# Kernel tuning notes

Hardware: AMD Instinct MI355X
Metric: run time of the kernel (lower is better)

The kernel has to match this reference:

```python
import jax, jax.numpy as jnp
import numpy as np

K, C, H, W, B = 128, 128, 24, 8, 32
HW = H * W
EPS = 1e-5


def setup_inputs() -> dict:
    key = jax.random.key(0)
    ks = jax.random.split(key, 4)
    feature = jax.random.normal(ks[0], (B, C, H, W), dtype=jnp.float32)
    target = jax.random.randint(ks[1], (B,), 0, K, dtype=jnp.int64)
    class_memory = jax.random.normal(ks[2], (K, C, H, W), dtype=jnp.float32)
    bn_gamma = jnp.ones((1,), jnp.float32)
    bn_beta = jnp.zeros((1,), jnp.float32)
    fc_w = jax.random.normal(ks[3], (1, 2 * HW), dtype=jnp.float32) / np.sqrt(2 * HW)
    fc_b = jnp.zeros((1,), jnp.float32)
    logit_gamma = jnp.ones((1,), jnp.float32)
    logit_beta = jnp.zeros((1,), jnp.float32)
    return {"feature": feature, "target": target, "class_memory": class_memory,
            "bn_gamma": bn_gamma, "bn_beta": bn_beta, "fc_w": fc_w, "fc_b": fc_b,
            "logit_gamma": logit_gamma, "logit_beta": logit_beta}


def _bn_all(x, gamma, beta):
    # BatchNorm1d with 1 channel in training mode: stats over ALL elements
    mean = x.mean()
    var = ((x - mean) ** 2).mean()  # biased variance, as torch uses for normalization
    return (x - mean) * jax.lax.rsqrt(var + EPS) * gamma[0] + beta[0]


def reference(feature, target, class_memory, bn_gamma, bn_beta, fc_w, fc_b,
              logit_gamma, logit_beta):
    f = feature.reshape(B, C, HW)        # query: [B, C, hw]
    m = class_memory.reshape(K, C, HW)   # memory: [K, C, hw]
    # correlation volume: score[k,b,q,p] = sum_c f[b,c,q] * m[k,c,p]
    corr = jnp.einsum('bcq,kcp->kbqp', f, m)  # [K, B, hw, hw]
    # dual-axis max pooling: best-match over query locs and over memory locs
    score = jnp.concatenate([corr.max(axis=2), corr.max(axis=3)], axis=-1)  # [K,B,2hw]
    score = _bn_all(score, bn_gamma, bn_beta)
    # FC to single logit per (class, sample)
    logits = score.reshape(K * B, 2 * HW) @ fc_w.T + fc_b  # [K*B, 1]
    logits = logits.reshape(K, B).T                         # [B, K]
    logits = _bn_all(logits, logit_gamma, logit_beta)
    # focal binary cross-entropy with logits
    onehot = jax.nn.one_hot(target, K, dtype=logits.dtype)  # [B, K]
    bce = onehot * jax.nn.softplus(-logits) + (1.0 - onehot) * jax.nn.softplus(logits)
    prob = jax.nn.sigmoid(logits)
    weight = jnp.where(onehot > 0.5, 1.0 - prob, prob) ** 2
    loss = (bce * weight).sum(-1)  # [B]
    preds = jnp.argmax(logits, axis=1)
    acc = (preds == target).astype(jnp.float32)
    return loss, acc
```

## Files before the change

kernel.cpp:

```cpp
#include <hip/hip_runtime.h>
#include <math.h>

#define BB 32
#define CCH 128
#define KK 128
#define HWW 192
#define NKB (KK * BB)
#define P2 (2 * HWW)

typedef __attribute__((ext_vector_type(8))) __bf16 bf16x8;
typedef __attribute__((ext_vector_type(16))) float f32x16;

#define A_ELEMS (BB * 8 * 6 * 512)
#define B_ELEMS (KK * 16 * 6 * 512)

__global__ __launch_bounds__(256) void pack_kernel(
    const float* __restrict__ feature,
    const float* __restrict__ class_memory,
    __bf16* __restrict__ A2,
    __bf16* __restrict__ B2)
{
    int gid = blockIdx.x * 256 + threadIdx.x;
    if (gid < 98304) {
        int l = gid & 63;
        int r = gid >> 6;
        int t = r % 6;  r /= 6;
        int ks = r & 7;
        int e = r >> 3;
        const float* src = feature + (size_t)e * CCH * HWW;
        int c0 = ks * 16 + (l >> 5) * 8;
        int q  = t * 32 + (l & 31);
        bf16x8 v;
#pragma unroll
        for (int j = 0; j < 8; ++j) v[j] = (__bf16)src[(c0 + j) * HWW + q];
        *(bf16x8*)(A2 + ((size_t)(e * 8 + ks) * 6 + t) * 512 + l * 8) = v;
    } else {
        int g2 = gid - 98304;
        int l = g2 & 63;
        int r = g2 >> 6;
        int t = r % 6;  r /= 6;
        int ks = r & 7;
        int e = r >> 3;
        const float* src = class_memory + (size_t)e * CCH * HWW;
        int c0 = ks * 16 + (l >> 5) * 8;
        int q  = t * 32 + (l & 31);
        bf16x8 vh, vl;
#pragma unroll
        for (int j = 0; j < 8; ++j) {
            float x = src[(c0 + j) * HWW + q];
            __bf16 h = (__bf16)x;
            vh[j] = h;
            vl[j] = (__bf16)(x - (float)h);
        }
        __bf16* base = B2 + ((size_t)e * 16 + ks) * 3072 + t * 512 + l * 8;
        *(bf16x8*)base = vh;
        *(bf16x8*)(base + 8 * 3072) = vl;
    }
}

#define MFMA32(A, B, C) __builtin_amdgcn_mfma_f32_32x32x16_bf16((A), (B), (C), 0, 0, 0)

__global__ __launch_bounds__(768, 3) void corr_mfma(
    const __bf16* __restrict__ A2,
    const __bf16* __restrict__ B2,
    const float* __restrict__ fc_w,
    float* __restrict__ dot_sw,
    float* __restrict__ psum,
    float* __restrict__ psq)
{
    __shared__ __align__(16) __bf16 A_lds[8][6][64][8];
    __shared__ __align__(16) __bf16 Blo_lds[8][6][64][8];
    __shared__ float colpart[2][192];
    __shared__ float rowpart[6][192];
    __shared__ float scores[384];

    const int tid = threadIdx.x;
    const int l   = tid & 63;
    const int lc  = l & 31;
    const int w   = tid >> 6;
    const int wy  = w / 6;
    const int wx  = w % 6;

    const int bid   = blockIdx.x;
    const int xcd   = bid & 7;
    const int slot  = bid >> 3;
    const int k     = xcd * 16 + (slot >> 1);
    const int bhalf = slot & 1;

    const __bf16* bkbase = B2 + (size_t)k * 49152;
    bf16x8 bh[8];
#pragma unroll
    for (int g = 0; g < 8; ++g)
        bh[g] = *(const bf16x8*)(bkbase + g * 3072 + wx * 512 + l * 8);

    float fcw[6];
#pragma unroll
    for (int u = 0; u < 6; ++u) fcw[u] = fc_w[l + 64 * u];

    const char* lobase = (const char*)B2 + (size_t)k * 98304 + 49152;
    const char* abase  = (const char*)A2;
    char* lodst = (char*)&Blo_lds[0][0][0][0];
    char* adst  = (char*)&A_lds[0][0][0][0];
    const int woff = w * 1024 + l * 16;
    const int wbase = w * 1024;

    auto stageA = [&](int b) {
        const char* src = abase + (size_t)b * 49152;
#pragma unroll
        for (int i = 0; i < 4; ++i)
            __builtin_amdgcn_global_load_lds(
                (const __attribute__((address_space(1))) void*)(src + i * 12288 + woff),
                (__attribute__((address_space(3))) void*)(adst + i * 12288 + wbase),
                16, 0, 0);
    };
#pragma unroll
    for (int i = 0; i < 4; ++i)
        __builtin_amdgcn_global_load_lds(
            (const __attribute__((address_space(1))) void*)(lobase + i * 12288 + woff),
            (__attribute__((address_space(3))) void*)(lodst + i * 12288 + wbase),
            16, 0, 0);
    stageA(bhalf * 16);
    __syncthreads();

    for (int bi = 0; bi < 16; ++bi) {
        const int b = bhalf * 16 + bi;

        f32x16 acc[3], acc2[3];
#pragma unroll
        for (int i = 0; i < 3; ++i)
#pragma unroll
            for (int rr = 0; rr < 16; ++rr) { acc[i][rr] = 0.f; acc2[i][rr] = 0.f; }

#pragma unroll
        for (int g = 0; g < 8; ++g) {
            bf16x8 a0 = *(const bf16x8*)&A_lds[g][wy * 3 + 0][l][0];
            bf16x8 a1 = *(const bf16x8*)&A_lds[g][wy * 3 + 1][l][0];
            bf16x8 a2 = *(const bf16x8*)&A_lds[g][wy * 3 + 2][l][0];
            bf16x8 bl = *(const bf16x8*)&Blo_lds[g][wx][l][0];
            acc[0]  = MFMA32(a0, bh[g], acc[0]);
            acc[0]  = MFMA32(a0, bl,    acc[0]);
            acc[1]  = MFMA32(a1, bh[g], acc[1]);
            acc[1]  = MFMA32(a1, bl,    acc[1]);
            acc[2]  = MFMA32(a2, bh[g], acc[2]);
            acc[2]  = MFMA32(a2, bl,    acc[2]);
            acc2[0] = MFMA32(bh[g], a0, acc2[0]);
            acc2[0] = MFMA32(bl,    a0, acc2[0]);
            acc2[1] = MFMA32(bh[g], a1, acc2[1]);
            acc2[1] = MFMA32(bl,    a1, acc2[1]);
            acc2[2] = MFMA32(bh[g], a2, acc2[2]);
            acc2[2] = MFMA32(bl,    a2, acc2[2]);
        }

        float cmv = -INFINITY;
#pragma unroll
        for (int i = 0; i < 3; ++i)
#pragma unroll
            for (int rr = 0; rr < 16; ++rr) cmv = fmaxf(cmv, acc[i][rr]);
        cmv = fmaxf(cmv, __shfl_xor(cmv, 32));
        if (l < 32) colpart[wy][wx * 32 + lc] = cmv;

#pragma unroll
        for (int i = 0; i < 3; ++i) {
            float t = -INFINITY;
#pragma unroll
            for (int rr = 0; rr < 16; ++rr) t = fmaxf(t, acc2[i][rr]);
            t = fmaxf(t, __shfl_xor(t, 32));
            if (l < 32) rowpart[wx][(wy * 3 + i) * 32 + lc] = t;
        }
        __syncthreads();

        if (bi < 15) stageA(b + 1);

        if (tid < 192) {
            scores[tid] = fmaxf(colpart[0][tid], colpart[1][tid]);
        } else if (tid < 384) {
            int q = tid - 192;
            float v = rowpart[0][q];
#pragma unroll
            for (int x = 1; x < 6; ++x) v = fmaxf(v, rowpart[x][q]);
            scores[192 + q] = v;
        }
        __syncthreads();

        if (tid < 64) {
            float ds = 0.f, s1 = 0.f, s2 = 0.f;
#pragma unroll
            for (int u = 0; u < 6; ++u) {
                float s = scores[l + 64 * u];
                ds = fmaf(s, fcw[u], ds);
                s1 += s;
                s2 = fmaf(s, s, s2);
            }
            for (int off = 32; off > 0; off >>= 1) {
                ds += __shfl_down(ds, off);
                s1 += __shfl_down(s1, off);
                s2 += __shfl_down(s2, off);
            }
            if (tid == 0) {
                int kb = k * 32 + b;
                dot_sw[kb] = ds;
                psum[kb]   = s1;
                psq[kb]    = s2;
            }
        }
    }
}

__device__ __forceinline__ float softplusf(float x) {
    return fmaxf(x, 0.f) + log1pf(expf(-fabsf(x)));
}

__device__ __forceinline__ float block_sum1024(float v, float* tmp) {
    __syncthreads();
    for (int off = 32; off > 0; off >>= 1) v += __shfl_down(v, off);
    if ((threadIdx.x & 63) == 0) tmp[threadIdx.x >> 6] = v;
    __syncthreads();
    float r = 0.f;
#pragma unroll
    for (int i = 0; i < 16; ++i) r += tmp[i];
    return r;
}

__global__ __launch_bounds__(1024) void finalize_kernel(
    const float* __restrict__ dot_sw,
    const float* __restrict__ psum,
    const float* __restrict__ psq,
    const float* __restrict__ fc_w,
    const float* __restrict__ fc_b,
    const float* __restrict__ bn_gamma,
    const float* __restrict__ bn_beta,
    const float* __restrict__ logit_gamma,
    const float* __restrict__ logit_beta,
    const int* __restrict__ target,
    float* __restrict__ out)
{
    const int tid = threadIdx.x;
    __shared__ float l_s[NKB];
    __shared__ float tmp[16];

    float s1 = 0.f, s2 = 0.f, sw = 0.f;
#pragma unroll
    for (int u = 0; u < 4; ++u) {
        int i = tid + 1024 * u;
        s1 += psum[i];
        s2 += psq[i];
    }
    if (tid < P2) sw = fc_w[tid];

    float S1 = block_sum1024(s1, tmp);
    float S2 = block_sum1024(s2, tmp);
    float SW = block_sum1024(sw, tmp);

    const float N1 = (float)NKB * (float)P2;
    float mean1 = S1 / N1;
    float var1  = S2 / N1 - mean1 * mean1;
    float cA = bn_gamma[0] * rsqrtf(var1 + 1e-5f);
    float cB = (bn_beta[0] - cA * mean1) * SW + fc_b[0];

    float lr[4];
    float t1 = 0.f, t2 = 0.f;
#pragma unroll
    for (int u = 0; u < 4; ++u) {
        int i = tid + 1024 * u;
        lr[u] = fmaf(cA, dot_sw[i], cB);
        t1 += lr[u];
        t2 = fmaf(lr[u], lr[u], t2);
    }
    float T1 = block_sum1024(t1, tmp);
    float T2 = block_sum1024(t2, tmp);
    float mean2 = T1 / (float)NKB;
    float var2  = T2 / (float)NKB - mean2 * mean2;
    float cC = logit_gamma[0] * rsqrtf(var2 + 1e-5f);
    float cD = logit_beta[0] - mean2 * cC;

#pragma unroll
    for (int u = 0; u < 4; ++u) {
        int i = tid + 1024 * u;
        l_s[i] = fmaf(lr[u], cC, cD);
    }
    __syncthreads();

    const int b  = tid >> 5;
    const int tt = tid & 31;
    const int tgt = target[b];
    float loss  = 0.f;
    float bestv = -INFINITY;
    int   bestk = 0x7fffffff;
#pragma unroll
    for (int u = 0; u < 4; ++u) {
        int kk = tt + 32 * u;
        float lg = l_s[kk * BB + b];
        float prob = 1.f / (1.f + expf(-lg));
        bool pos = (kk == tgt);
        float wgt = pos ? (1.f - prob) : prob;
        float bce = pos ? softplusf(-lg) : softplusf(lg);
        loss += bce * wgt * wgt;
        if (lg > bestv) { bestv = lg; bestk = kk; }
        else if (lg == bestv && kk < bestk) bestk = kk;
    }
    for (int off = 16; off > 0; off >>= 1) {
        loss += __shfl_down(loss, off, 32);
        float ov = __shfl_down(bestv, off, 32);
        int   ok = __shfl_down(bestk, off, 32);
        if (ov > bestv) { bestv = ov; bestk = ok; }
        else if (ov == bestv && ok < bestk) bestk = ok;
    }
    if (tt == 0) {
        out[b]      = loss;
        out[BB + b] = (bestk == tgt) ? 1.f : 0.f;
    }
}

extern "C" void kernel_launch(void* const* d_in, const int* in_sizes, int n_in,
                              void* d_out, int out_size, void* d_ws, size_t ws_size,
                              hipStream_t stream)
{
    const float* feature      = (const float*)d_in[0];
    const int*   target       = (const int*)d_in[1];
    const float* class_memory = (const float*)d_in[2];
    const float* bn_gamma     = (const float*)d_in[3];
    const float* bn_beta      = (const float*)d_in[4];
    const float* fc_w         = (const float*)d_in[5];
    const float* fc_b         = (const float*)d_in[6];
    const float* logit_gamma  = (const float*)d_in[7];
    const float* logit_beta   = (const float*)d_in[8];
    float* out = (float*)d_out;

    __bf16* A2 = (__bf16*)d_ws;
    __bf16* B2 = A2 + A_ELEMS;
    float* dot_sw = (float*)(B2 + B_ELEMS);
    float* psum   = dot_sw + NKB;
    float* psq    = psum + NKB;

    pack_kernel<<<1920, 256, 0, stream>>>(feature, class_memory, A2, B2);
    corr_mfma<<<256, 768, 0, stream>>>(A2, B2, fc_w, dot_sw, psum, psq);
    finalize_kernel<<<1, 1024, 0, stream>>>(dot_sw, psum, psq, fc_w, fc_b,
                                            bn_gamma, bn_beta,
                                            logit_gamma, logit_beta,
                                            target, out);
}
```

Measured before the change: 198.8 us.

## Double-buffer A tiles, drop a barrier, fuse finalize via last-block atomic

Measured after the change: 207.7 us. 1.04x slower.

```diff
diff --git a/kernel.cpp b/kernel.cpp
--- a/kernel.cpp
+++ b/kernel.cpp
@@ -18,9 +18,11 @@
     const float* __restrict__ feature,
     const float* __restrict__ class_memory,
     __bf16* __restrict__ A2,
-    __bf16* __restrict__ B2)
+    __bf16* __restrict__ B2,
+    unsigned int* __restrict__ counter)
 {
     int gid = blockIdx.x * 256 + threadIdx.x;
+    if (gid == 0) counter[0] = 0;
     if (gid < 98304) {
         int l = gid & 63;
         int r = gid >> 6;
@@ -58,6 +60,21 @@
     }
 }
 
+__device__ __forceinline__ float softplusf(float x) {
+    return fmaxf(x, 0.f) + log1pf(expf(-fabsf(x)));
+}
+
+__device__ __forceinline__ float block_sum768(float v, float* tmp) {
+    __syncthreads();
+    for (int off = 32; off > 0; off >>= 1) v += __shfl_down(v, off);
+    if ((threadIdx.x & 63) == 0) tmp[threadIdx.x >> 6] = v;
+    __syncthreads();
+    float r = 0.f;
+#pragma unroll
+    for (int i = 0; i < 12; ++i) r += tmp[i];
+    return r;
+}
+
 #define MFMA32(A, B, C) __builtin_amdgcn_mfma_f32_32x32x16_bf16((A), (B), (C), 0, 0, 0)
 
 __global__ __launch_bounds__(768, 3) void corr_mfma(
@@ -66,13 +83,21 @@
     const float* __restrict__ fc_w,
     float* __restrict__ dot_sw,
     float* __restrict__ psum,
-    float* __restrict__ psq)
+    float* __restrict__ psq,
+    unsigned int* __restrict__ counter,
+    const float* __restrict__ fc_b,
+    const float* __restrict__ bn_gamma,
+    const float* __restrict__ bn_beta,
+    const float* __restrict__ logit_gamma,
+    const float* __restrict__ logit_beta,
+    const int* __restrict__ target,
+    float* __restrict__ out)
 {
-    __shared__ __align__(16) __bf16 A_lds[8][6][64][8];
+    __shared__ __align__(16) __bf16 A_lds[2][8][6][64][8];
     __shared__ __align__(16) __bf16 Blo_lds[8][6][64][8];
-    __shared__ float colpart[2][192];
-    __shared__ float rowpart[6][192];
-    __shared__ float scores[384];
+    __shared__ float colpart[2][2][192];
+    __shared__ float rowpart[2][6][192];
+    __shared__ int   lastflag_s;
 
     const int tid = threadIdx.x;
     const int l   = tid & 63;
@@ -97,33 +122,36 @@
 #pragma unroll
     for (int u = 0; u < 6; ++u) fcw[u] = fc_w[l + 64 * u];
 
-    const char* lobase = (const char*)B2 + (size_t)k * 98304 + 49152;
-    const char* abase  = (const char*)A2;
-    char* lodst = (char*)&Blo_lds[0][0][0][0];
-    char* adst  = (char*)&A_lds[0][0][0][0];
-    const int woff = w * 1024 + l * 16;
+    const int woff  = w * 1024 + l * 16;
     const int wbase = w * 1024;
 
-    auto stageA = [&](int b) {
-        const char* src = abase + (size_t)b * 49152;
+    auto stageA = [&](int buf2, int b) {
+        const char* src = (const char*)A2 + (size_t)b * 49152 + woff;
+        char* dst = (char*)&A_lds[buf2][0][0][0][0] + wbase;
 #pragma unroll
         for (int i = 0; i < 4; ++i)
             __builtin_amdgcn_global_load_lds(
-                (const __attribute__((address_space(1))) void*)(src + i * 12288 + woff),
-                (__attribute__((address_space(3))) void*)(adst + i * 12288 + wbase),
+                (const __attribute__((address_space(1))) void*)(src + i * 12288),
+                (__attribute__((address_space(3))) void*)(dst + i * 12288),
                 16, 0, 0);
     };
-#pragma unroll
-    for (int i = 0; i < 4; ++i)
-        __builtin_amdgcn_global_load_lds(
-            (const __attribute__((address_space(1))) void*)(lobase + i * 12288 + woff),
-            (__attribute__((address_space(3))) void*)(lodst + i * 12288 + wbase),
-            16, 0, 0);
-    stageA(bhalf * 16);
+    {
+        const char* src = (const char*)B2 + (size_t)k * 98304 + 49152 + woff;
+        char* dst = (char*)&Blo_lds[0][0][0][0] + wbase;
+#pragma unroll
+        for (int i = 0; i < 4; ++i)
+            __builtin_amdgcn_global_load_lds(
+                (const __attribute__((address_space(1))) void*)(src + i * 12288),
+                (__attribute__((address_space(3))) void*)(dst + i * 12288),
+                16, 0, 0);
+    }
+    stageA(0, bhalf * 16);
     __syncthreads();
 
     for (int bi = 0; bi < 16; ++bi) {
-        const int b = bhalf * 16 + bi;
+        const int buf = bi & 1;
+        const int b   = bhalf * 16 + bi;
+        if (bi < 15) stageA(buf ^ 1, b + 1);
 
         f32x16 acc[3], acc2[3];
 #pragma unroll
@@ -133,9 +161,9 @@
 
 #pragma unroll
         for (int g = 0; g < 8; ++g) {
-            bf16x8 a0 = *(const bf16x8*)&A_lds[g][wy * 3 + 0][l][0];
-            bf16x8 a1 = *(const bf16x8*)&A_lds[g][wy * 3 + 1][l][0];
-            bf16x8 a2 = *(const bf16x8*)&A_lds[g][wy * 3 + 2][l][0];
+            bf16x8 a0 = *(const bf16x8*)&A_lds[buf][g][wy * 3 + 0][l][0];
+            bf16x8 a1 = *(const bf16x8*)&A_lds[buf][g][wy * 3 + 1][l][0];
+            bf16x8 a2 = *(const bf16x8*)&A_lds[buf][g][wy * 3 + 2][l][0];
             bf16x8 bl = *(const bf16x8*)&Blo_lds[g][wx][l][0];
             acc[0]  = MFMA32(a0, bh[g], acc[0]);
             acc[0]  = MFMA32(a0, bl,    acc[0]);
@@ -157,7 +185,7 @@
 #pragma unroll
             for (int rr = 0; rr < 16; ++rr) cmv = fmaxf(cmv, acc[i][rr]);
         cmv = fmaxf(cmv, __shfl_xor(cmv, 32));
-        if (l < 32) colpart[wy][wx * 32 + lc] = cmv;
+        if (l < 32) colpart[buf][wy][wx * 32 + lc] = cmv;
 
 #pragma unroll
         for (int i = 0; i < 3; ++i) {
@@ -165,29 +193,28 @@
 #pragma unroll
             for (int rr = 0; rr < 16; ++rr) t = fmaxf(t, acc2[i][rr]);
             t = fmaxf(t, __shfl_xor(t, 32));
-            if (l < 32) rowpart[wx][(wy * 3 + i) * 32 + lc] = t;
-        }
+            if (l < 32) rowpart[buf][wx][(wy * 3 + i) * 32 + lc] = t;
+        }
+
         __syncthreads();
 
-        if (bi < 15) stageA(b + 1);
-
-        if (tid < 192) {
-            scores[tid] = fmaxf(colpart[0][tid], colpart[1][tid]);
-        } else if (tid < 384) {
-            int q = tid - 192;
-            float v = rowpart[0][q];
-#pragma unroll
-            for (int x = 1; x < 6; ++x) v = fmaxf(v, rowpart[x][q]);
-            scores[192 + q] = v;
-        }
-        __syncthreads();
-
-        if (tid < 64) {
+        if (w == 0) {
             float ds = 0.f, s1 = 0.f, s2 = 0.f;
 #pragma unroll
-            for (int u = 0; u < 6; ++u) {
-                float s = scores[l + 64 * u];
+            for (int u = 0; u < 3; ++u) {
+                int p = l + 64 * u;
+                float s = fmaxf(colpart[buf][0][p], colpart[buf][1][p]);
                 ds = fmaf(s, fcw[u], ds);
+                s1 += s;
+                s2 = fmaf(s, s, s2);
+            }
+#pragma unroll
+            for (int u = 0; u < 3; ++u) {
+                int q = l + 64 * u;
+                float s = rowpart[buf][0][q];
+#pragma unroll
+                for (int x = 1; x < 6; ++x) s = fmaxf(s, rowpart[buf][x][q]);
+                ds = fmaf(s, fcw[3 + u], ds);
                 s1 += s;
                 s2 = fmaf(s, s, s2);
             }
@@ -196,7 +223,7 @@
                 s1 += __shfl_down(s1, off);
                 s2 += __shfl_down(s2, off);
             }
-            if (tid == 0) {
+            if (l == 0) {
                 int kb = k * 32 + b;
                 dot_sw[kb] = ds;
                 psum[kb]   = s1;
@@ -204,52 +231,31 @@
             }
         }
     }
-}
-
-__device__ __forceinline__ float softplusf(float x) {
-    return fmaxf(x, 0.f) + log1pf(expf(-fabsf(x)));
-}
-
-__device__ __forceinline__ float block_sum1024(float v, float* tmp) {
-    __syncthreads();
-    for (int off = 32; off > 0; off >>= 1) v += __shfl_down(v, off);
-    if ((threadIdx.x & 63) == 0) tmp[threadIdx.x >> 6] = v;
-    __syncthreads();
-    float r = 0.f;
-#pragma unroll
-    for (int i = 0; i < 16; ++i) r += tmp[i];
-    return r;
-}
-
-__global__ __launch_bounds__(1024) void finalize_kernel(
-    const float* __restrict__ dot_sw,
-    const float* __restrict__ psum,
-    const float* __restrict__ psq,
-    const float* __restrict__ fc_w,
-    const float* __restrict__ fc_b,
-    const float* __restrict__ bn_gamma,
-    const float* __restrict__ bn_beta,
-    const float* __restrict__ logit_gamma,
-    const float* __restrict__ logit_beta,
-    const int* __restrict__ target,
-    float* __restrict__ out)
-{
-    const int tid = threadIdx.x;
-    __shared__ float l_s[NKB];
-    __shared__ float tmp[16];
+
+    __syncthreads();
+    if (tid == 0) {
+        __threadfence();
+        unsigned int old = atomicAdd(counter, 1u);
+        lastflag_s = (old == 255u) ? 1 : 0;
+    }
+    __syncthreads();
+    if (!lastflag_s) return;
+    __threadfence();
+
+    float* l_s = (float*)&A_lds[0][0][0][0][0];
+    float* tmp = l_s + NKB;
 
     float s1 = 0.f, s2 = 0.f, sw = 0.f;
 #pragma unroll
-    for (int u = 0; u < 4; ++u) {
-        int i = tid + 1024 * u;
-        s1 += psum[i];
-        s2 += psq[i];
+    for (int u = 0; u < 6; ++u) {
+        int i = tid + 768 * u;
+        if (i < NKB) { s1 += psum[i]; s2 += psq[i]; }
     }
     if (tid < P2) sw = fc_w[tid];
 
-    float S1 = block_sum1024(s1, tmp);
-    float S2 = block_sum1024(s2, tmp);
-    float SW = block_sum1024(sw, tmp);
+    float S1 = block_sum768(s1, tmp);
+    float S2 = block_sum768(s2, tmp);
+    float SW = block_sum768(sw, tmp);
 
     const float N1 = (float)NKB * (float)P2;
     float mean1 = S1 / N1;
@@ -257,57 +263,62 @@
     float cA = bn_gamma[0] * rsqrtf(var1 + 1e-5f);
     float cB = (bn_beta[0] - cA * mean1) * SW + fc_b[0];
 
-    float lr[4];
+    float lr[6];
     float t1 = 0.f, t2 = 0.f;
 #pragma unroll
-    for (int u = 0; u < 4; ++u) {
-        int i = tid + 1024 * u;
-        lr[u] = fmaf(cA, dot_sw[i], cB);
-        t1 += lr[u];
-        t2 = fmaf(lr[u], lr[u], t2);
-    }
-    float T1 = block_sum1024(t1, tmp);
-    float T2 = block_sum1024(t2, tmp);
+    for (int u = 0; u < 6; ++u) {
+        int i = tid + 768 * u;
+        if (i < NKB) {
+            lr[u] = fmaf(cA, dot_sw[i], cB);
+            t1 += lr[u];
+            t2 = fmaf(lr[u], lr[u], t2);
+        } else lr[u] = 0.f;
+    }
+    float T1 = block_sum768(t1, tmp);
+    float T2 = block_sum768(t2, tmp);
     float mean2 = T1 / (float)NKB;
     float var2  = T2 / (float)NKB - mean2 * mean2;
     float cC = logit_gamma[0] * rsqrtf(var2 + 1e-5f);
     float cD = logit_beta[0] - mean2 * cC;
 
 #pragma unroll
-    for (int u = 0; u < 4; ++u) {
-        int i = tid + 1024 * u;
-        l_s[i] = fmaf(lr[u], cC, cD);
-    }
-    __syncthreads();
-
-    const int b  = tid >> 5;
-    const int tt = tid & 31;
-    const int tgt = target[b];
-    float loss  = 0.f;
-    float bestv = -INFINITY;
-    int   bestk = 0x7fffffff;
-#pragma unroll
-    for (int u = 0; u < 4; ++u) {
-        int kk = tt + 32 * u;
-        float lg = l_s[kk * BB + b];
-        float prob = 1.f / (1.f + expf(-lg));
-        bool pos = (kk == tgt);
-        float wgt = pos ? (1.f - prob) : prob;
-        float bce = pos ? softplusf(-lg) : softplusf(lg);
-        loss += bce * wgt * wgt;
-        if (lg > bestv) { bestv = lg; bestk = kk; }
-        else if (lg == bestv && kk < bestk) bestk = kk;
-    }
-    for (int off = 16; off > 0; off >>= 1) {
-        loss += __shfl_down(loss, off, 32);
-        float ov = __shfl_down(bestv, off, 32);
-        int   ok = __shfl_down(bestk, off, 32);
-        if (ov > bestv) { bestv = ov; bestk = ok; }
-        else if (ov == bestv && ok < bestk) bestk = ok;
-    }
-    if (tt == 0) {
-        out[b]      = loss;
-        out[BB + b] = (bestk == tgt) ? 1.f : 0.f;
+    for (int u = 0; u < 6; ++u) {
+        int i = tid + 768 * u;
+        if (i < NKB) l_s[i] = fmaf(lr[u], cC, cD);
+    }
+    __syncthreads();
+
+    if (tid < 128) {
+        const int b  = tid >> 2;
+        const int tt = tid & 3;
+        const int tgt = target[b];
+        float loss  = 0.f;
+        float bestv = -INFINITY;
+        int   bestk = 0x7fffffff;
+#pragma unroll
+        for (int u = 0; u < 32; ++u) {
+            int kk = tt + 4 * u;
+            float lg = l_s[kk * BB + b];
+            float prob = 1.f / (1.f + expf(-lg));
+            bool pos = (kk == tgt);
+            float wgt = pos ? (1.f - prob) : prob;
+            float bce = pos ? softplusf(-lg) : softplusf(lg);
+            loss += bce * wgt * wgt;
+            if (lg > bestv) { bestv = lg; bestk = kk; }
+            else if (lg == bestv && kk < bestk) bestk = kk;
+        }
+#pragma unroll
+        for (int off = 2; off > 0; off >>= 1) {
+            loss += __shfl_down(loss, off);
+            float ov = __shfl_down(bestv, off);
+            int   ok = __shfl_down(bestk, off);
+            if (ov > bestv) { bestv = ov; bestk = ok; }
+            else if (ov == bestv && ok < bestk) bestk = ok;
+        }
+        if (tt == 0) {
+            out[b]      = loss;
+            out[BB + b] = (bestk == tgt) ? 1.f : 0.f;
+        }
     }
 }
 
@@ -331,11 +342,10 @@
     float* dot_sw = (float*)(B2 + B_ELEMS);
     float* psum   = dot_sw + NKB;
     float* psq    = psum + NKB;
-
-    pack_kernel<<<1920, 256, 0, stream>>>(feature, class_memory, A2, B2);
-    corr_mfma<<<256, 768, 0, stream>>>(A2, B2, fc_w, dot_sw, psum, psq);
-    finalize_kernel<<<1, 1024, 0, stream>>>(dot_sw, psum, psq, fc_w, fc_b,
-                                            bn_gamma, bn_beta,
-                                            logit_gamma, logit_beta,
-                                            target, out);
-}
+    unsigned int* counter = (unsigned int*)(psq + NKB);
+
+    pack_kernel<<<1920, 256, 0, stream>>>(feature, class_memory, A2, B2, counter);
+    corr_mfma<<<256, 768, 0, stream>>>(A2, B2, fc_w, dot_sw, psum, psq, counter,
+                                       fc_b, bn_gamma, bn_beta,
+                                       logit_gamma, logit_beta, target, out);
+}
```
